# Performance work log

Measured on AMD Instinct MI355X. Metric: run time of the kernel, lower is better.

## Reference

```python
import jax, jax.numpy as jnp
import numpy as np
from jax import lax

EPS = 1e-5  # torch BatchNorm2d default eps
Q = 28      # patch size; 3 VALID 3x3 convs -> 22x22
FC_IN = 128 * 22 * 22


def _conv_bn_relu(x, w, b, g, be, m, v):
    # x: (N, Cin, H, W), w: (Cout, Cin, 3, 3) -- VALID conv + inference BN + ReLU
    y = lax.conv_general_dilated(x, w, (1, 1), 'VALID',
                                 dimension_numbers=('NCHW', 'OIHW', 'NCHW'))
    scale = (g / jnp.sqrt(v + EPS))[None, :, None, None]
    shift = (be - (m - b) * g / jnp.sqrt(v + EPS))[None, :, None, None]
    # equivalent to ((y + b) - m)/sqrt(v+eps)*g + be
    return jax.nn.relu(y * scale + shift)


def _conv_params(key, cin, cout):
    k = jax.random.split(key, 6)
    w = jax.random.normal(k[0], (cout, cin, 3, 3), jnp.float32) / np.sqrt(cin * 9)
    b = 0.01 * jax.random.normal(k[1], (cout,), jnp.float32)
    g = 1.0 + 0.1 * jax.random.normal(k[2], (cout,), jnp.float32)
    be = 0.1 * jax.random.normal(k[3], (cout,), jnp.float32)
    m = 0.1 * jax.random.normal(k[4], (cout,), jnp.float32)
    v = jax.random.uniform(k[5], (cout,), jnp.float32, 0.5, 1.5)
    return w, b, g, be, m, v


def setup_inputs() -> dict:
    key = jax.random.key(0)
    kx, k1, k2, k3, kf = jax.random.split(key, 5)
    x = jax.random.normal(kx, (128, 1, 84, 84), jnp.float32)
    w1, b1, g1, be1, m1, v1 = _conv_params(k1, 1, 64)
    w2, b2, g2, be2, m2, v2 = _conv_params(k2, 64, 64)
    w3, b3, g3, be3, m3, v3 = _conv_params(k3, 64, 128)
    kfw, kfb = jax.random.split(kf)
    wf = jax.random.normal(kfw, (100, FC_IN), jnp.float32) / np.sqrt(FC_IN)
    bf = 0.01 * jax.random.normal(kfb, (100,), jnp.float32)
    return dict(x=x,
                w1=w1, b1=b1, g1=g1, be1=be1, m1=m1, v1=v1,
                w2=w2, b2=b2, g2=g2, be2=be2, m2=m2, v2=v2,
                w3=w3, b3=b3, g3=g3, be3=be3, m3=m3, v3=v3,
                wf=wf, bf=bf)


def reference(x, w1, b1, g1, be1, m1, v1,
              w2, b2, g2, be2, m2, v2,
              w3, b3, g3, be3, m3, v3,
              wf, bf):
    B = x.shape[0]
    # img_to_patch: (B,1,84,84) -> 3x3 grid of (1,28,28) patches, index (i=W-block, j=H-block)
    p = x.reshape(B, 1, 3, Q, 3, Q).transpose(0, 2, 4, 1, 3, 5).reshape(B * 9, 1, Q, Q)
    h = _conv_bn_relu(p, w1, b1, g1, be1, m1, v1)   # (B*9, 64, 26, 26)
    h = _conv_bn_relu(h, w2, b2, g2, be2, m2, v2)   # (B*9, 64, 24, 24)
    h = _conv_bn_relu(h, w3, b3, g3, be3, m3, v3)   # (B*9, 128, 22, 22)
    out = h.reshape(B * 9, FC_IN) @ wf.T + bf       # (B*9, 100)
    return out.reshape(B, 3, 3, 100)
```

## Files before the change

### kernel.cpp

```cpp
#include <hip/hip_runtime.h>
#include <hip/hip_fp16.h>

#define EPS 1e-5f

typedef _Float16 f16x8 __attribute__((ext_vector_type(8)));
typedef float f32x4 __attribute__((ext_vector_type(4)));

#define WFHT_OFF 0ull
#define W2P_OFF 7929856ull
#define W3P_OFF 7966720ull
#define H3_OFF  8040448ull
#define FOLD_OFF 79409152ull

__device__ __forceinline__ uint32_t pk2(float a, float b) {
    __half2 h = __floats2half2_rn(a, b);
    return *reinterpret_cast<uint32_t*>(&h);
}

__global__ __launch_bounds__(256)
void k_prep(const float* __restrict__ w1, const float* __restrict__ b1,
            const float* __restrict__ g1, const float* __restrict__ be1,
            const float* __restrict__ m1, const float* __restrict__ v1,
            const float* __restrict__ w2, const float* __restrict__ b2,
            const float* __restrict__ g2, const float* __restrict__ be2,
            const float* __restrict__ m2, const float* __restrict__ v2,
            const float* __restrict__ w3, const float* __restrict__ b3,
            const float* __restrict__ g3, const float* __restrict__ be3,
            const float* __restrict__ m3, const float* __restrict__ v3,
            const float* __restrict__ wf, const float* __restrict__ bf,
            __half* __restrict__ ws, float* __restrict__ out)
{
    const int i = blockIdx.x * 256 + threadIdx.x;
    float* fold = reinterpret_cast<float*>(ws + FOLD_OFF);
    if (i < 247808) {
        const int ks = i >> 7, o = i & 127;
        uint2 pk[8];
        if (o < 100) {
            const float* src = wf + (size_t)o * 61952 + ks * 32;
            #pragma unroll
            for (int t = 0; t < 8; ++t) {
                const float4 f = *reinterpret_cast<const float4*>(src + 4 * t);
                pk[t] = make_uint2(pk2(f.x, f.y), pk2(f.z, f.w));
            }
        } else {
            #pragma unroll
            for (int t = 0; t < 8; ++t) pk[t] = make_uint2(0u, 0u);
        }
        uint2* dst = reinterpret_cast<uint2*>(ws + WFHT_OFF + (size_t)i * 32);
        #pragma unroll
        for (int t = 0; t < 8; ++t) dst[t] = pk[t];
    } else if (i < 284672) {
        const int j = i - 247808;
        const int kk = j >> 11, rem = j & 2047;
        const int co = rem >> 5, kl = rem & 31;
        const int tap = kk >> 1, ci = (kk & 1) * 32 + kl;
        const float sc = g2[co] * rsqrtf(v2[co] + EPS);
        ws[W2P_OFF + j] = __float2half(w2[co * 576 + ci * 9 + tap] * sc);
    } else if (i < 358400) {
        const int j = i - 284672;
        const int wn = j / 36864, r = j % 36864;
        const int kk = r >> 11, rem = r & 2047;
        const int col = rem >> 5, kl = rem & 31;
        const int co = wn * 64 + col;
        const int tap = kk >> 1, ci = (kk & 1) * 32 + kl;
        const float sc = g3[co] * rsqrtf(v3[co] + EPS);
        ws[W3P_OFF + j] = __float2half(w3[co * 576 + ci * 9 + tap] * sc);
    } else if (i < 473600) {
        const int j = i - 358400;
        out[j] = bf[j % 100];
    } else if (i < 474432) {
        const int j = i - 473600;
        if (j < 576) {
            const int co = j / 9;
            fold[j] = w1[j] * (g1[co] * rsqrtf(v1[co] + EPS));
        } else if (j < 640) {
            const int co = j - 576;
            const float sc = g1[co] * rsqrtf(v1[co] + EPS);
            fold[j] = be1[co] - (m1[co] - b1[co]) * sc;
        } else if (j < 704) {
            const int co = j - 640;
            const float sc = g2[co] * rsqrtf(v2[co] + EPS);
            fold[j] = be2[co] - (m2[co] - b2[co]) * sc;
        } else {
            const int co = j - 704;
            const float sc = g3[co] * rsqrtf(v3[co] + EPS);
            fold[j] = be3[co] - (m3[co] - b3[co]) * sc;
        }
    }
}

__device__ __forceinline__ int lds128(int row, int colByte) {
    return row * 128 + (colByte ^ ((row & 7) << 4));
}

__global__ __launch_bounds__(512, 2)
void k_conv123(const float* __restrict__ x, const __half* __restrict__ ws_c,
               __half* __restrict__ ws)
{
    __shared__ char smem[51824];
    float* patch = reinterpret_cast<float*>(smem);
    char* act = smem + 1904;

    const int bid = blockIdx.x;
    const int p = bid >> 1, half = bid & 1;
    const int tid = threadIdx.x, lane = tid & 63, wave = tid >> 6;
    const int l15 = lane & 15, g = lane >> 4;
    const int wm = wave >> 1, wn = wave & 1;
    const int base3 = half * 11;
    const float* fold = reinterpret_cast<const float*>(ws_c + FOLD_OFF);

    {
        const int b = p / 9, r9 = p - b * 9, hb = r9 / 3, wb = r9 - hb * 3;
        const float* xb = x + (size_t)b * 7056 + (hb * 28 + base3) * 84 + wb * 28;
        if (tid < 476) patch[tid] = xb[(tid / 28) * 84 + (tid % 28)];
    }
    __syncthreads();

    {
        const int co = lane;
        float wr[9];
        #pragma unroll
        for (int t = 0; t < 9; ++t) wr[t] = fold[co * 9 + t];
        const float sh = fold[576 + co];
        #pragma unroll
        for (int rr = 0; rr < 2; ++rr) {
            const int r = wave * 2 + rr;
            if (r < 15) {
                const float* prow = patch + r * 28;
                float a0 = prow[0], a1 = prow[28], a2 = prow[56];
                float b0 = prow[1], b1 = prow[29], b2 = prow[57];
                for (int xp = 0; xp < 13; ++xp) {
                    const int xx = xp * 2;
                    const float2 c0 = *reinterpret_cast<const float2*>(prow + xx + 2);
                    const float2 c1 = *reinterpret_cast<const float2*>(prow + xx + 30);
                    const float2 c2 = *reinterpret_cast<const float2*>(prow + xx + 58);
                    float s = a0 * wr[0] + b0 * wr[1] + c0.x * wr[2]
                            + a1 * wr[3] + b1 * wr[4] + c1.x * wr[5]
                            + a2 * wr[6] + b2 * wr[7] + c2.x * wr[8];
                    *reinterpret_cast<__half*>(act + lds128(r * 26 + xx, co * 2)) =
                        __float2half(fmaxf(s + sh, 0.f));
                    s = b0 * wr[0] + c0.x * wr[1] + c0.y * wr[2]
                      + b1 * wr[3] + c1.x * wr[4] + c1.y * wr[5]
                      + b2 * wr[6] + c2.x * wr[7] + c2.y * wr[8];
                    *reinterpret_cast<__half*>(act + lds128(r * 26 + xx + 1, co * 2)) =
                        __float2half(fmaxf(s + sh, 0.f));
                    a0 = c0.x; a1 = c1.x; a2 = c2.x;
                    b0 = c0.y; b1 = c1.y; b2 = c2.y;
                }
            }
        }
    }
    __syncthreads();

    int rb2[5];
    #pragma unroll
    for (int t = 0; t < 5; ++t) {
        int m = (wm * 5 + t) * 16 + l15;
        if (m > 311) m = 311;
        const int yy = m / 24, xx = m - yy * 24;
        rb2[t] = yy * 26 + xx;
    }
    f32x4 acc2[5][2];
    #pragma unroll
    for (int t = 0; t < 5; ++t)
        #pragma unroll
        for (int ct = 0; ct < 2; ++ct) acc2[t][ct] = (f32x4)0.f;

    {
        const __half* w2w = ws_c + W2P_OFF + wn * 1024 + l15 * 32 + g * 8;
        #pragma unroll
        for (int tap = 0; tap < 9; ++tap) {
            const int ro = (tap / 3) * 26 + (tap % 3);
            int ad[5];
            #pragma unroll
            for (int t = 0; t < 5; ++t) ad[t] = lds128(rb2[t] + ro, g * 16);
            #pragma unroll
            for (int par = 0; par < 2; ++par) {
                const int kk = tap * 2 + par;
                const f16x8 wv0 = *reinterpret_cast<const f16x8*>(w2w + kk * 2048);
                const f16x8 wv1 = *reinterpret_cast<const f16x8*>(w2w + kk * 2048 + 512);
                #pragma unroll
                for (int t = 0; t < 5; ++t) {
                    const f16x8 af = *reinterpret_cast<const f16x8*>(act + (ad[t] ^ (par * 64)));
                    acc2[t][0] = __builtin_amdgcn_mfma_f32_16x16x32_f16(wv0, af, acc2[t][0], 0, 0, 0);
                    acc2[t][1] = __builtin_amdgcn_mfma_f32_16x16x32_f16(wv1, af, acc2[t][1], 0, 0, 0);
                }
            }
        }
    }
    __syncthreads();

    {
        #pragma unroll
        for (int ct = 0; ct < 2; ++ct) {
            const int co0 = wn * 32 + ct * 16 + g * 4;
            const float4 sh4 = *reinterpret_cast<const float4*>(fold + 640 + co0);
            #pragma unroll
            for (int t = 0; t < 5; ++t) {
                const int m = (wm * 5 + t) * 16 + l15;
                if (m < 312) {
                    const float v0 = fmaxf(acc2[t][ct][0] + sh4.x, 0.f);
                    const float v1 = fmaxf(acc2[t][ct][1] + sh4.y, 0.f);
                    const float v2_ = fmaxf(acc2[t][ct][2] + sh4.z, 0.f);
                    const float v3_ = fmaxf(acc2[t][ct][3] + sh4.w, 0.f);
                    *reinterpret_cast<uint2*>(
                        act + lds128(m, wn * 64 + ct * 32 + g * 8)) =
                        make_uint2(pk2(v0, v1), pk2(v2_, v3_));
                }
            }
        }
    }
    __syncthreads();

    int rb3[4];
    #pragma unroll
    for (int t = 0; t < 4; ++t) {
        int m = (wm * 4 + t) * 16 + l15;
        if (m > 241) m = 241;
        const int yy = m / 22, xx = m - yy * 22;
        rb3[t] = yy * 24 + xx;
    }
    f32x4 acc3[4][4];
    #pragma unroll
    for (int t = 0; t < 4; ++t)
        #pragma unroll
        for (int ct = 0; ct < 4; ++ct) acc3[t][ct] = (f32x4)0.f;

    {
        const __half* w3w = ws_c + W3P_OFF + wn * 36864 + l15 * 32 + g * 8;
        #pragma unroll
        for (int tap = 0; tap < 9; ++tap) {
            const int ro = (tap / 3) * 24 + (tap % 3);
            int ad[4];
            #pragma unroll
            for (int t = 0; t < 4; ++t) ad[t] = lds128(rb3[t] + ro, g * 16);
            #pragma unroll
            for (int par = 0; par < 2; ++par) {
                const int kk = tap * 2 + par;
                f16x8 wv[4];
                #pragma unroll
                for (int ct = 0; ct < 4; ++ct)
                    wv[ct] = *reinterpret_cast<const f16x8*>(w3w + kk * 2048 + ct * 512);
                #pragma unroll
                for (int t = 0; t < 4; ++t) {
                    const f16x8 af = *reinterpret_cast<const f16x8*>(act + (ad[t] ^ (par * 64)));
                    #pragma unroll
                    for (int ct = 0; ct < 4; ++ct)
                        acc3[t][ct] = __builtin_amdgcn_mfma_f32_16x16x32_f16(
                            wv[ct], af, acc3[t][ct], 0, 0, 0);
                }
            }
        }
    }

    {
        __half* slot = ws + H3_OFF + (size_t)p * 61952;
        #pragma unroll
        for (int ct = 0; ct < 4; ++ct) {
            const int co0 = wn * 64 + ct * 16 + g * 4;
            const float4 sh4 = *reinterpret_cast<const float4*>(fold + 704 + co0);
            #pragma unroll
            for (int t = 0; t < 4; ++t) {
                const int m = (wm * 4 + t) * 16 + l15;
                if (m < 242) {
                    const int pixg = 242 * half + m;
                    slot[(size_t)(co0 + 0) * 484 + pixg] =
                        __float2half(fmaxf(acc3[t][ct][0] + sh4.x, 0.f));
                    slot[(size_t)(co0 + 1) * 484 + pixg] =
                        __float2half(fmaxf(acc3[t][ct][1] + sh4.y, 0.f));
                    slot[(size_t)(co0 + 2) * 484 + pixg] =
                        __float2half(fmaxf(acc3[t][ct][2] + sh4.z, 0.f));
                    slot[(size_t)(co0 + 3) * 484 + pixg] =
                        __float2half(fmaxf(acc3[t][ct][3] + sh4.w, 0.f));
                }
            }
        }
    }
}

__global__ __launch_bounds__(256)
void k_fc(const __half* __restrict__ ws, float* __restrict__ out)
{
    const __half* h3 = ws + H3_OFF;
    __shared__ char As[2][16384];

    const int bid = blockIdx.x;
    const int mb = bid % 18, kc = bid / 18;
    const int tid = threadIdx.x, lane = tid & 63, wave = tid >> 6;
    const int wm = wave >> 1, wn = wave & 1;
    const int l15 = lane & 15, g = lane >> 4;

    const size_t kbase = (size_t)kc * 1408;

    const int srow = tid >> 4;
    const int scolB = (tid & 15) * 16;
    const __half* sbase = h3 + (size_t)(mb * 64) * 61952 + kbase + (tid & 15) * 8;

    const __half* Bp[4];
    #pragma unroll
    for (int nt = 0; nt < 4; ++nt)
        Bp[nt] = ws + WFHT_OFF + (size_t)(kc * 44) * 4096
               + (size_t)(wn * 64 + nt * 16 + l15) * 32 + g * 8;

    f32x4 acc[2][4];
    #pragma unroll
    for (int mt = 0; mt < 2; ++mt)
        #pragma unroll
        for (int nt = 0; nt < 4; ++nt) acc[mt][nt] = (f32x4)0.f;

    {
        uint4 sv[4];
        #pragma unroll
        for (int pp = 0; pp < 4; ++pp)
            sv[pp] = *reinterpret_cast<const uint4*>(sbase + (size_t)(pp * 16 + srow) * 61952);
        #pragma unroll
        for (int pp = 0; pp < 4; ++pp) {
            const int row = pp * 16 + srow;
            *reinterpret_cast<uint4*>(As[0] + row * 256 + (scolB ^ ((row & 7) << 4))) = sv[pp];
        }
    }

    for (int s = 0; s < 11; ++s) {
        __syncthreads();

        uint4 sv[4];
        const int nb = (s + 1) & 1;
        if (s < 10) {
            #pragma unroll
            for (int pp = 0; pp < 4; ++pp)
                sv[pp] = *reinterpret_cast<const uint4*>(
                    sbase + (size_t)(pp * 16 + srow) * 61952 + (s + 1) * 128);
        }

        const char* Ab = As[s & 1];
        #pragma unroll
        for (int kk = 0; kk < 4; ++kk) {
            f16x8 a[2];
            #pragma unroll
            for (int mt = 0; mt < 2; ++mt) {
                const int row = wm * 32 + mt * 16 + l15;
                a[mt] = *reinterpret_cast<const f16x8*>(
                    Ab + row * 256 + ((kk * 64 + g * 16) ^ ((row & 7) << 4)));
            }
            f16x8 b[4];
            #pragma unroll
            for (int nt = 0; nt < 4; ++nt)
                b[nt] = *reinterpret_cast<const f16x8*>(Bp[nt] + (s * 4 + kk) * 4096);
            #pragma unroll
            for (int nt = 0; nt < 4; ++nt) {
                acc[0][nt] = __builtin_amdgcn_mfma_f32_16x16x32_f16(a[0], b[nt], acc[0][nt], 0, 0, 0);
                acc[1][nt] = __builtin_amdgcn_mfma_f32_16x16x32_f16(a[1], b[nt], acc[1][nt], 0, 0, 0);
            }
        }

        if (s < 10) {
            #pragma unroll
            for (int pp = 0; pp < 4; ++pp) {
                const int row = pp * 16 + srow;
                *reinterpret_cast<uint4*>(As[nb] + row * 256 + (scolB ^ ((row & 7) << 4))) = sv[pp];
            }
        }
    }

    #pragma unroll
    for (int mt = 0; mt < 2; ++mt)
        #pragma unroll
        for (int nt = 0; nt < 4; ++nt) {
            const int col = wn * 64 + nt * 16 + l15;
            if (col < 100) {
                #pragma unroll
                for (int r = 0; r < 4; ++r) {
                    const int row = mb * 64 + wm * 32 + mt * 16 + g * 4 + r;
                    atomicAdd(out + (size_t)row * 100 + col, acc[mt][nt][r]);
                }
            }
        }
}

extern "C" void kernel_launch(void* const* d_in, const int* in_sizes, int n_in,
                              void* d_out, int out_size, void* d_ws, size_t ws_size,
                              hipStream_t stream)
{
    const float* x   = (const float*)d_in[0];
    const float* w1  = (const float*)d_in[1];
    const float* b1  = (const float*)d_in[2];
    const float* g1  = (const float*)d_in[3];
    const float* be1 = (const float*)d_in[4];
    const float* m1  = (const float*)d_in[5];
    const float* v1  = (const float*)d_in[6];
    const float* w2  = (const float*)d_in[7];
    const float* b2  = (const float*)d_in[8];
    const float* g2  = (const float*)d_in[9];
    const float* be2 = (const float*)d_in[10];
    const float* m2  = (const float*)d_in[11];
    const float* v2  = (const float*)d_in[12];
    const float* w3  = (const float*)d_in[13];
    const float* b3  = (const float*)d_in[14];
    const float* g3  = (const float*)d_in[15];
    const float* be3 = (const float*)d_in[16];
    const float* m3  = (const float*)d_in[17];
    const float* v3  = (const float*)d_in[18];
    const float* wf  = (const float*)d_in[19];
    const float* bf  = (const float*)d_in[20];

    __half* hws = (__half*)d_ws;
    float* out = (float*)d_out;

    k_prep<<<1854, 256, 0, stream>>>(w1, b1, g1, be1, m1, v1,
                                     w2, b2, g2, be2, m2, v2,
                                     w3, b3, g3, be3, m3, v3,
                                     wf, bf, hws, out);
    k_conv123<<<2304, 512, 0, stream>>>(x, hws, hws);
    k_fc<<<792, 256, 0, stream>>>(hws, out);
}
```

Measured before the change: 245.5 us.

## Stage conv2/conv3 weights into LDS via async global_load_lds triple buffering

Conv2 and conv3 weight fragments were previously loaded per wave straight from global memory inside the MFMA loops. They are now staged cooperatively into a three-slot LDS ring buffer with global_load_lds, using vmcnt waits and workgroup barriers to prefetch two stages ahead. The conv3 weight layout is repacked so each K-slice is contiguous, and launch bounds are raised to 4 waves per EU. The cost is extra LDS (76 KB per block, which limits occupancy) and a barrier per stage that may stall waves.

```diff
diff --git a/kernel.cpp b/kernel.cpp
--- a/kernel.cpp
+++ b/kernel.cpp
@@ -5,10 +5,12 @@
 
 typedef _Float16 f16x8 __attribute__((ext_vector_type(8)));
 typedef float f32x4 __attribute__((ext_vector_type(4)));
+typedef __attribute__((address_space(3))) uint32_t lds_u32;
+typedef const __attribute__((address_space(1))) uint32_t glb_u32;
 
 #define WFHT_OFF 0ull
 #define W2P_OFF 7929856ull
-#define W3P_OFF 7966720ull
+#define W3Q_OFF 7966720ull
 #define H3_OFF  8040448ull
 #define FOLD_OFF 79409152ull
 
@@ -58,13 +60,11 @@
         ws[W2P_OFF + j] = __float2half(w2[co * 576 + ci * 9 + tap] * sc);
     } else if (i < 358400) {
         const int j = i - 284672;
-        const int wn = j / 36864, r = j % 36864;
-        const int kk = r >> 11, rem = r & 2047;
-        const int col = rem >> 5, kl = rem & 31;
-        const int co = wn * 64 + col;
+        const int kk = j >> 12, rem = j & 4095;
+        const int co = rem >> 5, kl = rem & 31;
         const int tap = kk >> 1, ci = (kk & 1) * 32 + kl;
         const float sc = g3[co] * rsqrtf(v3[co] + EPS);
-        ws[W3P_OFF + j] = __float2half(w3[co * 576 + ci * 9 + tap] * sc);
+        ws[W3Q_OFF + j] = __float2half(w3[co * 576 + ci * 9 + tap] * sc);
     } else if (i < 473600) {
         const int j = i - 358400;
         out[j] = bf[j % 100];
@@ -93,13 +93,14 @@
     return row * 128 + (colByte ^ ((row & 7) << 4));
 }
 
-__global__ __launch_bounds__(512, 2)
+__global__ __launch_bounds__(512, 4)
 void k_conv123(const float* __restrict__ x, const __half* __restrict__ ws_c,
                __half* __restrict__ ws)
 {
-    __shared__ char smem[51824];
+    __shared__ char smem[76400];
     float* patch = reinterpret_cast<float*>(smem);
     char* act = smem + 1904;
+    char* wbuf = smem + 51824;
 
     const int bid = blockIdx.x;
     const int p = bid >> 1, half = bid & 1;
@@ -152,6 +153,9 @@
     }
     __syncthreads();
 
+    const __half* w2q = ws_c + W2P_OFF;
+    const __half* w3q = ws_c + W3Q_OFF;
+
     int rb2[5];
     #pragma unroll
     for (int t = 0; t < 5; ++t) {
@@ -167,18 +171,30 @@
         for (int ct = 0; ct < 2; ++ct) acc2[t][ct] = (f32x4)0.f;
 
     {
-        const __half* w2w = ws_c + W2P_OFF + wn * 1024 + l15 * 32 + g * 8;
+        const int w2off = wn * 2048 + l15 * 64 + g * 16;
+        #define STG2(TAP)                                                          \
+            __builtin_amdgcn_global_load_lds(                                      \
+                (glb_u32*)(w2q + (TAP) * 4096 + wave * 512 + lane * 8),            \
+                (lds_u32*)(wbuf + ((TAP) % 3) * 8192 + wave * 1024), 16, 0, 0)
+        STG2(0); STG2(1); STG2(2);
         #pragma unroll
         for (int tap = 0; tap < 9; ++tap) {
+            if (tap == 0)      asm volatile("s_waitcnt vmcnt(2)" ::: "memory");
+            else if (tap < 8)  asm volatile("s_waitcnt vmcnt(1)" ::: "memory");
+            else               asm volatile("s_waitcnt vmcnt(0)" ::: "memory");
+            __builtin_amdgcn_sched_barrier(0);
+            __builtin_amdgcn_s_barrier();
+            __builtin_amdgcn_sched_barrier(0);
+            if (tap >= 1 && tap <= 6) STG2(tap + 2);
+            const char* sb = wbuf + (tap % 3) * 8192;
             const int ro = (tap / 3) * 26 + (tap % 3);
             int ad[5];
             #pragma unroll
             for (int t = 0; t < 5; ++t) ad[t] = lds128(rb2[t] + ro, g * 16);
             #pragma unroll
             for (int par = 0; par < 2; ++par) {
-                const int kk = tap * 2 + par;
-                const f16x8 wv0 = *reinterpret_cast<const f16x8*>(w2w + kk * 2048);
-                const f16x8 wv1 = *reinterpret_cast<const f16x8*>(w2w + kk * 2048 + 512);
+                const f16x8 wv0 = *reinterpret_cast<const f16x8*>(sb + par * 4096 + w2off);
+                const f16x8 wv1 = *reinterpret_cast<const f16x8*>(sb + par * 4096 + w2off + 1024);
                 #pragma unroll
                 for (int t = 0; t < 5; ++t) {
                     const f16x8 af = *reinterpret_cast<const f16x8*>(act + (ad[t] ^ (par * 64)));
@@ -187,6 +203,7 @@
                 }
             }
         }
+        #undef STG2
     }
     __syncthreads();
 
@@ -227,7 +244,12 @@
         for (int ct = 0; ct < 4; ++ct) acc3[t][ct] = (f32x4)0.f;
 
     {
-        const __half* w3w = ws_c + W3P_OFF + wn * 36864 + l15 * 32 + g * 8;
+        const int w3off = wn * 4096 + l15 * 64 + g * 16;
+        #define STG3(KK)                                                           \
+            __builtin_amdgcn_global_load_lds(                                      \
+                (glb_u32*)(w3q + (KK) * 4096 + wave * 512 + lane * 8),             \
+                (lds_u32*)(wbuf + ((KK) % 3) * 8192 + wave * 1024), 16, 0, 0)
+        STG3(0); STG3(1); STG3(2);
         #pragma unroll
         for (int tap = 0; tap < 9; ++tap) {
             const int ro = (tap / 3) * 24 + (tap % 3);
@@ -237,13 +259,22 @@
             #pragma unroll
             for (int par = 0; par < 2; ++par) {
                 const int kk = tap * 2 + par;
+                if (kk == 0)       asm volatile("s_waitcnt vmcnt(2)" ::: "memory");
+                else if (kk < 17)  asm volatile("s_waitcnt vmcnt(1)" ::: "memory");
+                else               asm volatile("s_waitcnt vmcnt(0)" ::: "memory");
+                __builtin_amdgcn_sched_barrier(0);
+                __builtin_amdgcn_s_barrier();
+                __builtin_amdgcn_sched_barrier(0);
+                if (kk >= 1 && kk <= 15) STG3(kk + 2);
+                const char* sb = wbuf + (kk % 3) * 8192;
                 f16x8 wv[4];
                 #pragma unroll
                 for (int ct = 0; ct < 4; ++ct)
-                    wv[ct] = *reinterpret_cast<const f16x8*>(w3w + kk * 2048 + ct * 512);
+                    wv[ct] = *reinterpret_cast<const f16x8*>(sb + w3off + ct * 1024);
+                const int px = par * 64;
                 #pragma unroll
                 for (int t = 0; t < 4; ++t) {
-                    const f16x8 af = *reinterpret_cast<const f16x8*>(act + (ad[t] ^ (par * 64)));
+                    const f16x8 af = *reinterpret_cast<const f16x8*>(act + (ad[t] ^ px));
                     #pragma unroll
                     for (int ct = 0; ct < 4; ++ct)
                         acc3[t][ct] = __builtin_amdgcn_mfma_f32_16x16x32_f16(
@@ -251,6 +282,7 @@
                 }
             }
         }
+        #undef STG3
     }
 
     {
```

Measured after the change: 234.8 us. 4.4% less time.
